# Kernel tuning notes

Hardware: AMD Instinct MI355X
Metric: run time of the kernel (lower is better)

## Reference

```python
import jax, jax.numpy as jnp
import numpy as np

H = W = 56      # image resolution
WS = 7          # window size
SS = 3          # shift size
NH = 8          # num heads
E = 256         # embed dim
HD = E // NH    # head dim (qkv Linear operates per-head on HD)
NW = (H // WS) * (W // WS)  # 64 windows
WD = WS * WS                # 49 tokens per window


def _rel_pos_index():
    coords = np.stack(np.meshgrid(np.arange(WS), np.arange(WS), indexing='ij'))  # (2,WS,WS)
    cf = coords.reshape(2, -1)
    rel = (cf[:, :, None] - cf[:, None, :]).transpose(1, 2, 0)  # (WD,WD,2)
    rel[..., 0] += WS - 1
    rel[..., 1] += WS - 1
    rel[..., 0] *= 2 * WS - 1
    return rel.sum(-1)  # (WD,WD) ints in [0, (2WS-1)^2)


def _attn_mask():
    # Swin shifted-window attention mask: -100 where tokens come from different regions.
    m = np.zeros((H, W))
    slices = (slice(0, -WS), slice(-WS, -SS), slice(-SS, None))
    cnt = 0
    for hs in slices:
        for ws in slices:
            m[hs, ws] = cnt
            cnt += 1
    mw = m.reshape(H // WS, WS, W // WS, WS).transpose(0, 2, 1, 3).reshape(NW, WD)
    diff = mw[:, None, :] - mw[:, :, None]  # (NW,WD,WD)
    return np.where(diff != 0, -100.0, 0.0).astype(np.float32)


def setup_inputs() -> dict:
    key = jax.random.key(0)
    ks = jax.random.split(key, 6)
    return {
        'x': jax.random.normal(ks[0], (32, H * W, E), jnp.float32),
        'qkv_w': jax.random.normal(ks[1], (HD, 3 * HD), jnp.float32) * 0.05,
        'qkv_b': jax.random.normal(ks[2], (3 * HD,), jnp.float32) * 0.05,
        'proj_w': jax.random.normal(ks[3], (E, E), jnp.float32) * 0.05,
        'proj_b': jax.random.normal(ks[4], (E,), jnp.float32) * 0.05,
        'rpb_table': jax.random.normal(ks[5], ((2 * WS - 1) ** 2, NH), jnp.float32) * 0.02,
    }


def reference(x, qkv_w, qkv_b, proj_w, proj_b, rpb_table):
    B = x.shape[0]
    rpi = _rel_pos_index()
    bias = rpb_table[rpi.reshape(-1)].reshape(WD, WD, NH).transpose(2, 0, 1)  # (NH,WD,WD)
    mask = jnp.asarray(_attn_mask())  # (NW,WD,WD)

    xs = x.reshape(B, H, W, E)
    xs = jnp.roll(xs, (-SS, -SS), axis=(1, 2))  # cyclic shift (equals cycle_shift)
    # window partition -> (B,NW,WD,E)
    xw = xs.reshape(B, H // WS, WS, W // WS, WS, E).transpose(0, 1, 3, 2, 4, 5).reshape(B, NW, WD, E)
    # split heads -> (B,NW,NH,WD,HD)
    xh = xw.reshape(B, NW, WD, NH, HD).transpose(0, 1, 3, 2, 4)
    qkv = xh @ qkv_w + qkv_b  # per-head shared qkv projection (as in original)
    q, k, v = jnp.split(qkv, 3, axis=-1)
    scores = jnp.einsum('bwhqd,bwhkd->bwhqk', q, k) / np.sqrt(HD).astype(np.float32)
    scores = scores + bias + mask[None, :, None]  # (B,NW,NH,WD,WD)
    attn = jax.nn.softmax(scores, axis=-1)
    o = jnp.einsum('bwhqk,bwhkd->bwhqd', attn, v)
    # merge heads and reverse window partition
    o = o.transpose(0, 1, 3, 2, 4).reshape(B, NW, WD, E)
    o = o.reshape(B, H // WS, W // WS, WS, WS, E).transpose(0, 1, 3, 2, 4, 5).reshape(B, H, W, E)
    o = jnp.roll(o, (SS, SS), axis=(1, 2)).reshape(B, H * W, E)  # reverse cyclic shift
    return o @ proj_w + proj_b
```

## Files before the change

### kernel.cpp

```cpp
#include <hip/hip_runtime.h>
#include <hip/hip_bf16.h>

#define WSZ 7
#define WD  49
#define NH  8
#define NWIN 64
#define HH  56
#define SS  3
#define TOK 3136
#define EMB 256

typedef __attribute__((ext_vector_type(8))) short bf16x8;
typedef __attribute__((ext_vector_type(8))) unsigned short u16x8;
typedef __attribute__((ext_vector_type(4))) float f32x4;

#define OFF_WT   0
#define OFF_BIAS 7680
#define OFF_RPB  8064
#define OFF_REG  13472
#define OFF_POS  13728
#define OFF_PW   13984
#define PW_SZ    14848
#define PW_K     5120
#define PW_VT    10240
#define LDS_TOTAL (OFF_PW + 4*PW_SZ)

__device__ __forceinline__ unsigned short f2bf(float f) {
    union { float f; unsigned u; } v; v.f = f;
    return (unsigned short)((v.u + 0x7FFFu + ((v.u >> 16) & 1u)) >> 16);
}
__device__ __forceinline__ unsigned long long pack4(float a, float b, float c, float d) {
    return (unsigned long long)f2bf(a) | ((unsigned long long)f2bf(b) << 16)
         | ((unsigned long long)f2bf(c) << 32) | ((unsigned long long)f2bf(d) << 48);
}

__global__ __launch_bounds__(256, 1) void attn_kernel(
    const float* __restrict__ x, const float* __restrict__ qkv_w,
    const float* __restrict__ qkv_b, const float* __restrict__ rpb,
    unsigned short* __restrict__ o_mid)
{
    extern __shared__ char smem[];
    unsigned short* sWT = (unsigned short*)(smem + OFF_WT);
    float* sBias = (float*)(smem + OFF_BIAS);
    float* sRPB  = (float*)(smem + OFF_RPB);
    int*   sREG  = (int*)(smem + OFF_REG);
    int*   sPOS  = (int*)(smem + OFF_POS);

    const int tid = threadIdx.x;
    const int w = blockIdx.x & 63, b = blockIdx.x >> 6;
    const int wi = w >> 3, wj = w & 7;

    if (tid < 64) {
        int ti = tid / 7, tj = tid - (tid / 7) * 7;
        int sh = wi * WSZ + ti, sw = wj * WSZ + tj;
        int rr = (sh < HH - WSZ) ? 0 : (sh < HH - SS) ? 1 : 2;
        int rc = (sw < HH - WSZ) ? 0 : (sw < HH - SS) ? 1 : 2;
        sREG[tid] = rr * 3 + rc;
        sPOS[tid] = ((sh + SS) % HH) * HH + ((sw + SS) % HH);
    }
    for (int i = tid; i < 32 * 96; i += 256) {
        int c = i / 96, j = i - c * 96;
        sWT[j * 40 + c] = f2bf(qkv_w[i]);
    }
    for (int i = tid; i < 96; i += 256) sBias[i] = qkv_b[i];
    for (int i = tid; i < 169 * NH; i += 256) sRPB[i] = rpb[i];
    __syncthreads();

    const int wave = tid >> 6, lane = tid & 63;
    const int cl = lane & 15, quad = lane >> 4;
    unsigned short* sQ  = (unsigned short*)(smem + OFF_PW + wave * PW_SZ);
    unsigned short* sK  = sQ + PW_K / 2;
    unsigned short* sVT = sQ + PW_VT / 2;
    unsigned short* sP  = sQ;

    const float* xrow[4];
    #pragma unroll
    for (int mt = 0; mt < 4; ++mt) {
        int tok = mt * 16 + cl;
        xrow[mt] = x + ((size_t)b * TOK + sPOS[tok]) * EMB + quad * 8;
    }
    int ki[4], kj[4], kreg[4];
    #pragma unroll
    for (int nt = 0; nt < 4; ++nt) {
        int kt = nt * 16 + cl;
        ki[nt] = kt / 7; kj[nt] = kt - ki[nt] * 7;
        kreg[nt] = sREG[kt];
    }
    const float qscale = 0.17677669529663687f;

    #pragma unroll
    for (int hi = 0; hi < 2; ++hi) {
        const int h = wave * 2 + hi;
        bf16x8 xa[4];
        #pragma unroll
        for (int mt = 0; mt < 4; ++mt) {
            const float* p = xrow[mt] + h * 32;
            float4 v0 = *(const float4*)p, v1 = *(const float4*)(p + 4);
            union { bf16x8 v; unsigned long long q[2]; } u;
            u.q[0] = pack4(v0.x, v0.y, v0.z, v0.w);
            u.q[1] = pack4(v1.x, v1.y, v1.z, v1.w);
            xa[mt] = u.v;
        }
        #pragma unroll
        for (int nt = 0; nt < 6; ++nt) {
            bf16x8 wb = *(const bf16x8*)(&sWT[(nt * 16 + cl) * 40 + quad * 8]);
            float bias = sBias[nt * 16 + cl];
            #pragma unroll
            for (int mt = 0; mt < 4; ++mt) {
                f32x4 c = {bias, bias, bias, bias};
                c = __builtin_amdgcn_mfma_f32_16x16x32_bf16(xa[mt], wb, c, 0, 0, 0);
                int tok0 = mt * 16 + quad * 4;
                if (nt < 2) {
                    int col = nt * 16 + cl;
                    #pragma unroll
                    for (int r = 0; r < 4; ++r)
                        sQ[(tok0 + r) * 40 + col] = f2bf(c[r] * qscale);
                } else if (nt < 4) {
                    int col = nt * 16 + cl - 32;
                    #pragma unroll
                    for (int r = 0; r < 4; ++r)
                        sK[(tok0 + r) * 40 + col] = f2bf(c[r]);
                } else {
                    int hd = nt * 16 + cl - 64;
                    *(unsigned long long*)(&sVT[hd * 72 + tok0]) =
                        pack4(c[0], c[1], c[2], c[3]);
                }
            }
        }
        bf16x8 qa[4], kb[4];
        #pragma unroll
        for (int mt = 0; mt < 4; ++mt) qa[mt] = *(const bf16x8*)(&sQ[(mt * 16 + cl) * 40 + quad * 8]);
        #pragma unroll
        for (int nt = 0; nt < 4; ++nt) kb[nt] = *(const bf16x8*)(&sK[(nt * 16 + cl) * 40 + quad * 8]);
        f32x4 sc[4][4];
        #pragma unroll
        for (int mt = 0; mt < 4; ++mt)
            #pragma unroll
            for (int nt = 0; nt < 4; ++nt) {
                f32x4 z = {0.f, 0.f, 0.f, 0.f};
                sc[mt][nt] = __builtin_amdgcn_mfma_f32_16x16x32_bf16(qa[mt], kb[nt], z, 0, 0, 0);
            }
        #pragma unroll
        for (int mt = 0; mt < 4; ++mt) {
            #pragma unroll
            for (int r = 0; r < 4; ++r) {
                int qt = mt * 16 + quad * 4 + r;
                int qi = qt / 7, qj = qt - qi * 7;
                int qreg = sREG[qt];
                float pv[4], sm = 0.f;
                #pragma unroll
                for (int nt = 0; nt < 4; ++nt) {
                    int kt = nt * 16 + cl;
                    float v = sc[mt][nt][r];
                    int idx = (qi - ki[nt] + 6) * 13 + (qj - kj[nt] + 6);
                    idx = idx < 0 ? 0 : (idx > 168 ? 168 : idx);
                    v += sRPB[idx * NH + h];
                    if (kreg[nt] != qreg) v -= 100.f;
                    if (kt >= WD) v = -1e30f;
                    v = __expf(v);
                    pv[nt] = v; sm += v;
                }
                sm += __shfl_xor(sm, 1, 16);
                sm += __shfl_xor(sm, 2, 16);
                sm += __shfl_xor(sm, 4, 16);
                sm += __shfl_xor(sm, 8, 16);
                float inv = 1.f / sm;
                #pragma unroll
                for (int nt = 0; nt < 4; ++nt)
                    sP[qt * 72 + nt * 16 + cl] = f2bf(pv[nt] * inv);
            }
        }
        f32x4 ot[2][4];
        #pragma unroll
        for (int mv = 0; mv < 2; ++mv)
            #pragma unroll
            for (int nt = 0; nt < 4; ++nt) ot[mv][nt] = (f32x4){0.f, 0.f, 0.f, 0.f};
        #pragma unroll
        for (int ks = 0; ks < 2; ++ks) {
            bf16x8 va[2], pb[4];
            #pragma unroll
            for (int mv = 0; mv < 2; ++mv)
                va[mv] = *(const bf16x8*)(&sVT[(mv * 16 + cl) * 72 + ks * 32 + quad * 8]);
            #pragma unroll
            for (int nt = 0; nt < 4; ++nt)
                pb[nt] = *(const bf16x8*)(&sP[(nt * 16 + cl) * 72 + ks * 32 + quad * 8]);
            #pragma unroll
            for (int mv = 0; mv < 2; ++mv)
                #pragma unroll
                for (int nt = 0; nt < 4; ++nt)
                    ot[mv][nt] = __builtin_amdgcn_mfma_f32_16x16x32_bf16(va[mv], pb[nt], ot[mv][nt], 0, 0, 0);
        }
        #pragma unroll
        for (int nt = 0; nt < 4; ++nt) {
            int qt = nt * 16 + cl;
            if (qt < WD) {
                int pos = sPOS[qt];
                unsigned short* dst = o_mid + ((size_t)b * TOK + pos) * EMB + h * 32 + quad * 4;
                *(unsigned long long*)(dst)      = pack4(ot[0][nt][0], ot[0][nt][1], ot[0][nt][2], ot[0][nt][3]);
                *(unsigned long long*)(dst + 16) = pack4(ot[1][nt][0], ot[1][nt][1], ot[1][nt][2], ot[1][nt][3]);
            }
        }
    }
}

__global__ __launch_bounds__(256) void cvt_kernel(
    const float* __restrict__ W, unsigned short* __restrict__ Wt)
{
    int i = blockIdx.x * 256 + threadIdx.x;
    int k = i >> 8, n = i & 255;
    Wt[n * 256 + k] = f2bf(W[i]);
}

__global__ __launch_bounds__(256) void proj_kernel(
    const unsigned short* __restrict__ A,
    const unsigned short* __restrict__ Wt,
    const float* __restrict__ bias, float* __restrict__ C, int M)
{
    alignas(16) __shared__ unsigned short sA[128 * 32];
    alignas(16) __shared__ unsigned short sB[128 * 32];
    const int tid = threadIdx.x;
    const int wave = tid >> 6, lane = tid & 63;
    const int cl = lane & 15, quad = lane >> 4;
    const int wx = wave & 1, wy = wave >> 1;
    const size_t m0 = (size_t)blockIdx.x * 128;
    const int n0 = blockIdx.y * 128;

    float bias_r[4];
    #pragma unroll
    for (int nt = 0; nt < 4; ++nt) bias_r[nt] = bias[n0 + wx * 64 + nt * 16 + cl];

    f32x4 acc[4][4];
    #pragma unroll
    for (int mt = 0; mt < 4; ++mt)
        #pragma unroll
        for (int nt = 0; nt < 4; ++nt) acc[mt][nt] = (f32x4){0.f, 0.f, 0.f, 0.f};

    for (int k0 = 0; k0 < 256; k0 += 32) {
        #pragma unroll
        for (int s = 0; s < 2; ++s) {
            int c = s * 256 + tid;
            int row = c >> 2, ch = c & 3;
            *(u16x8*)(sA + row * 32 + ch * 8) = *(const u16x8*)(A  + (m0 + row) * 256 + k0 + ch * 8);
            *(u16x8*)(sB + row * 32 + ch * 8) = *(const u16x8*)(Wt + (size_t)(n0 + row) * 256 + k0 + ch * 8);
        }
        __syncthreads();
        bf16x8 af[4], bf[4];
        #pragma unroll
        for (int mt = 0; mt < 4; ++mt) af[mt] = *(const bf16x8*)(&sA[(wy * 64 + mt * 16 + cl) * 32 + quad * 8]);
        #pragma unroll
        for (int nt = 0; nt < 4; ++nt) bf[nt] = *(const bf16x8*)(&sB[(wx * 64 + nt * 16 + cl) * 32 + quad * 8]);
        #pragma unroll
        for (int mt = 0; mt < 4; ++mt)
            #pragma unroll
            for (int nt = 0; nt < 4; ++nt)
                acc[mt][nt] = __builtin_amdgcn_mfma_f32_16x16x32_bf16(af[mt], bf[nt], acc[mt][nt], 0, 0, 0);
        __syncthreads();
    }
    #pragma unroll
    for (int mt = 0; mt < 4; ++mt)
        #pragma unroll
        for (int nt = 0; nt < 4; ++nt) {
            #pragma unroll
            for (int r = 0; r < 4; ++r) {
                size_t m = m0 + wy * 64 + mt * 16 + quad * 4 + r;
                int n = n0 + wx * 64 + nt * 16 + cl;
                C[m * 256 + n] = acc[mt][nt][r] + bias_r[nt];
            }
        }
}

extern "C" void kernel_launch(void* const* d_in, const int* in_sizes, int n_in,
                              void* d_out, int out_size, void* d_ws, size_t ws_size,
                              hipStream_t stream) {
    const float* x      = (const float*)d_in[0];
    const float* qkv_w  = (const float*)d_in[1];
    const float* qkv_b  = (const float*)d_in[2];
    const float* proj_w = (const float*)d_in[3];
    const float* proj_b = (const float*)d_in[4];
    const float* rpb    = (const float*)d_in[5];
    float* out = (float*)d_out;

    const int B = in_sizes[0] / (TOK * EMB);
    const int M = B * TOK;

    unsigned short* o_mid = (unsigned short*)d_ws;
    unsigned short* Wt    = (unsigned short*)((char*)d_ws + (size_t)M * EMB * 2);

    (void)hipFuncSetAttribute(reinterpret_cast<const void*>(&attn_kernel),
                              hipFuncAttributeMaxDynamicSharedMemorySize, LDS_TOTAL);
    cvt_kernel<<<256, 256, 0, stream>>>(proj_w, Wt);
    attn_kernel<<<B * NWIN, 256, LDS_TOTAL, stream>>>(x, qkv_w, qkv_b, rpb, o_mid);
    dim3 g(M / 128, EMB / 128);
    proj_kernel<<<g, 256, 0, stream>>>(o_mid, Wt, proj_b, out, M);
}
```

Baseline: 290.9 us.

## Fuse output projection into windowed attention kernel

The per-head attention outputs of each window are kept in registers, staged as bf16 into shared memory, and multiplied by the projection weights inside the same kernel, with bias added and results scattered straight to the output. This removes the bf16 intermediate round trip through global memory and the separate projection GEMM launch. In exchange each block reads the full 256x256 bf16 weight matrix from global/L2 with no LDS reuse, and more accumulators stay live, which raises register pressure. Launch bounds also change to request two blocks per CU, which may not fit the LDS budget.

```diff
diff --git a/kernel.cpp b/kernel.cpp
--- a/kernel.cpp
+++ b/kernel.cpp
@@ -24,6 +24,7 @@
 #define PW_K     5120
 #define PW_VT    10240
 #define LDS_TOTAL (OFF_PW + 4*PW_SZ)
+#define SO_STRIDE 264
 
 __device__ __forceinline__ unsigned short f2bf(float f) {
     union { float f; unsigned u; } v; v.f = f;
@@ -34,10 +35,12 @@
          | ((unsigned long long)f2bf(c) << 32) | ((unsigned long long)f2bf(d) << 48);
 }
 
-__global__ __launch_bounds__(256, 1) void attn_kernel(
+__global__ __launch_bounds__(256, 2) void fused_kernel(
     const float* __restrict__ x, const float* __restrict__ qkv_w,
     const float* __restrict__ qkv_b, const float* __restrict__ rpb,
-    unsigned short* __restrict__ o_mid)
+    const unsigned short* __restrict__ Wt,
+    const float* __restrict__ proj_b,
+    float* __restrict__ out)
 {
     extern __shared__ char smem[];
     unsigned short* sWT = (unsigned short*)(smem + OFF_WT);
@@ -87,6 +90,8 @@
         kreg[nt] = sREG[kt];
     }
     const float qscale = 0.17677669529663687f;
+
+    f32x4 otr[2][2][4];
 
     #pragma unroll
     for (int hi = 0; hi < 2; ++hi) {
@@ -170,11 +175,10 @@
                     sP[qt * 72 + nt * 16 + cl] = f2bf(pv[nt] * inv);
             }
         }
-        f32x4 ot[2][4];
         #pragma unroll
         for (int mv = 0; mv < 2; ++mv)
             #pragma unroll
-            for (int nt = 0; nt < 4; ++nt) ot[mv][nt] = (f32x4){0.f, 0.f, 0.f, 0.f};
+            for (int nt = 0; nt < 4; ++nt) otr[hi][mv][nt] = (f32x4){0.f, 0.f, 0.f, 0.f};
         #pragma unroll
         for (int ks = 0; ks < 2; ++ks) {
             bf16x8 va[2], pb[4];
@@ -188,16 +192,59 @@
             for (int mv = 0; mv < 2; ++mv)
                 #pragma unroll
                 for (int nt = 0; nt < 4; ++nt)
-                    ot[mv][nt] = __builtin_amdgcn_mfma_f32_16x16x32_bf16(va[mv], pb[nt], ot[mv][nt], 0, 0, 0);
-        }
-        #pragma unroll
-        for (int nt = 0; nt < 4; ++nt) {
-            int qt = nt * 16 + cl;
-            if (qt < WD) {
-                int pos = sPOS[qt];
-                unsigned short* dst = o_mid + ((size_t)b * TOK + pos) * EMB + h * 32 + quad * 4;
-                *(unsigned long long*)(dst)      = pack4(ot[0][nt][0], ot[0][nt][1], ot[0][nt][2], ot[0][nt][3]);
-                *(unsigned long long*)(dst + 16) = pack4(ot[1][nt][0], ot[1][nt][1], ot[1][nt][2], ot[1][nt][3]);
+                    otr[hi][mv][nt] = __builtin_amdgcn_mfma_f32_16x16x32_bf16(va[mv], pb[nt], otr[hi][mv][nt], 0, 0, 0);
+        }
+    }
+
+    __syncthreads();
+    unsigned short* sO = (unsigned short*)(smem + OFF_PW);
+    #pragma unroll
+    for (int hi = 0; hi < 2; ++hi) {
+        const int h = wave * 2 + hi;
+        #pragma unroll
+        for (int mv = 0; mv < 2; ++mv)
+            #pragma unroll
+            for (int nt = 0; nt < 4; ++nt) {
+                int qt = nt * 16 + cl;
+                f32x4 o = otr[hi][mv][nt];
+                *(unsigned long long*)(&sO[qt * SO_STRIDE + h * 32 + mv * 16 + quad * 4]) =
+                    pack4(o[0], o[1], o[2], o[3]);
+            }
+    }
+    __syncthreads();
+
+    const int n0 = wave * 64;
+    f32x4 acc[4][4];
+    #pragma unroll
+    for (int mt = 0; mt < 4; ++mt)
+        #pragma unroll
+        for (int tt = 0; tt < 4; ++tt) acc[mt][tt] = (f32x4){0.f, 0.f, 0.f, 0.f};
+    #pragma unroll
+    for (int ks = 0; ks < 8; ++ks) {
+        bf16x8 wa[4], ob[4];
+        #pragma unroll
+        for (int mt = 0; mt < 4; ++mt)
+            wa[mt] = *(const bf16x8*)(Wt + (size_t)(n0 + mt * 16 + cl) * 256 + ks * 32 + quad * 8);
+        #pragma unroll
+        for (int tt = 0; tt < 4; ++tt)
+            ob[tt] = *(const bf16x8*)(&sO[(tt * 16 + cl) * SO_STRIDE + ks * 32 + quad * 8]);
+        #pragma unroll
+        for (int mt = 0; mt < 4; ++mt)
+            #pragma unroll
+            for (int tt = 0; tt < 4; ++tt)
+                acc[mt][tt] = __builtin_amdgcn_mfma_f32_16x16x32_bf16(wa[mt], ob[tt], acc[mt][tt], 0, 0, 0);
+    }
+    #pragma unroll
+    for (int mt = 0; mt < 4; ++mt) {
+        float4 bq = *(const float4*)(proj_b + n0 + mt * 16 + quad * 4);
+        #pragma unroll
+        for (int tt = 0; tt < 4; ++tt) {
+            int tok = tt * 16 + cl;
+            if (tok < WD) {
+                f32x4 v = acc[mt][tt];
+                v[0] += bq.x; v[1] += bq.y; v[2] += bq.z; v[3] += bq.w;
+                float* dst = out + ((size_t)b * TOK + sPOS[tok]) * EMB + n0 + mt * 16 + quad * 4;
+                *(f32x4*)dst = v;
             }
         }
     }
@@ -209,64 +256,6 @@
     int i = blockIdx.x * 256 + threadIdx.x;
     int k = i >> 8, n = i & 255;
     Wt[n * 256 + k] = f2bf(W[i]);
-}
-
-__global__ __launch_bounds__(256) void proj_kernel(
-    const unsigned short* __restrict__ A,
-    const unsigned short* __restrict__ Wt,
-    const float* __restrict__ bias, float* __restrict__ C, int M)
-{
-    alignas(16) __shared__ unsigned short sA[128 * 32];
-    alignas(16) __shared__ unsigned short sB[128 * 32];
-    const int tid = threadIdx.x;
-    const int wave = tid >> 6, lane = tid & 63;
-    const int cl = lane & 15, quad = lane >> 4;
-    const int wx = wave & 1, wy = wave >> 1;
-    const size_t m0 = (size_t)blockIdx.x * 128;
-    const int n0 = blockIdx.y * 128;
-
-    float bias_r[4];
-    #pragma unroll
-    for (int nt = 0; nt < 4; ++nt) bias_r[nt] = bias[n0 + wx * 64 + nt * 16 + cl];
-
-    f32x4 acc[4][4];
-    #pragma unroll
-    for (int mt = 0; mt < 4; ++mt)
-        #pragma unroll
-        for (int nt = 0; nt < 4; ++nt) acc[mt][nt] = (f32x4){0.f, 0.f, 0.f, 0.f};
-
-    for (int k0 = 0; k0 < 256; k0 += 32) {
-        #pragma unroll
-        for (int s = 0; s < 2; ++s) {
-            int c = s * 256 + tid;
-            int row = c >> 2, ch = c & 3;
-            *(u16x8*)(sA + row * 32 + ch * 8) = *(const u16x8*)(A  + (m0 + row) * 256 + k0 + ch * 8);
-            *(u16x8*)(sB + row * 32 + ch * 8) = *(const u16x8*)(Wt + (size_t)(n0 + row) * 256 + k0 + ch * 8);
-        }
-        __syncthreads();
-        bf16x8 af[4], bf[4];
-        #pragma unroll
-        for (int mt = 0; mt < 4; ++mt) af[mt] = *(const bf16x8*)(&sA[(wy * 64 + mt * 16 + cl) * 32 + quad * 8]);
-        #pragma unroll
-        for (int nt = 0; nt < 4; ++nt) bf[nt] = *(const bf16x8*)(&sB[(wx * 64 + nt * 16 + cl) * 32 + quad * 8]);
-        #pragma unroll
-        for (int mt = 0; mt < 4; ++mt)
-            #pragma unroll
-            for (int nt = 0; nt < 4; ++nt)
-                acc[mt][nt] = __builtin_amdgcn_mfma_f32_16x16x32_bf16(af[mt], bf[nt], acc[mt][nt], 0, 0, 0);
-        __syncthreads();
-    }
-    #pragma unroll
-    for (int mt = 0; mt < 4; ++mt)
-        #pragma unroll
-        for (int nt = 0; nt < 4; ++nt) {
-            #pragma unroll
-            for (int r = 0; r < 4; ++r) {
-                size_t m = m0 + wy * 64 + mt * 16 + quad * 4 + r;
-                int n = n0 + wx * 64 + nt * 16 + cl;
-                C[m * 256 + n] = acc[mt][nt][r] + bias_r[nt];
-            }
-        }
 }
 
 extern "C" void kernel_launch(void* const* d_in, const int* in_sizes, int n_in,
@@ -281,15 +270,11 @@
     float* out = (float*)d_out;
 
     const int B = in_sizes[0] / (TOK * EMB);
-    const int M = B * TOK;
-
-    unsigned short* o_mid = (unsigned short*)d_ws;
-    unsigned short* Wt    = (unsigned short*)((char*)d_ws + (size_t)M * EMB * 2);
-
-    (void)hipFuncSetAttribute(reinterpret_cast<const void*>(&attn_kernel),
+
+    unsigned short* Wt = (unsigned short*)d_ws;
+
+    (void)hipFuncSetAttribute(reinterpret_cast<const void*>(&fused_kernel),
                               hipFuncAttributeMaxDynamicSharedMemorySize, LDS_TOTAL);
     cvt_kernel<<<256, 256, 0, stream>>>(proj_w, Wt);
-    attn_kernel<<<B * NWIN, 256, LDS_TOTAL, stream>>>(x, qkv_w, qkv_b, rpb, o_mid);
-    dim3 g(M / 128, EMB / 128);
-    proj_kernel<<<g, 256, 0, stream>>>(o_mid, Wt, proj_b, out, M);
-}
+    fused_kernel<<<B * NWIN, 256, LDS_TOTAL, stream>>>(x, qkv_w, qkv_b, rpb, Wt, proj_b, out);
+}
```

New measurement: 298.1 us. 1.02x slower.
